# Kernel tuning notes

Measured on AMD Instinct MI355X. Metric: run time of the kernel, lower is better.

The kernel has to match this reference:

```python
import jax, jax.numpy as jnp
import numpy as np

N, DQ, T, H1 = 131072, 256, 4, 512

def setup_inputs() -> dict:
    key = jax.random.key(0)
    k_q, k_w0, k_b0, k_w1, k_z = jax.random.split(key, 5)
    return {
        "q": jax.random.normal(k_q, (N, DQ), dtype=jnp.float32),
        "Z": jax.random.randint(k_z, (N,), 0, T, dtype=jnp.int32),
        "W0": jax.random.normal(k_w0, (T, DQ, H1), dtype=jnp.float32) * (1.0 / np.sqrt(DQ)),
        "b0": jax.random.normal(k_b0, (T, H1), dtype=jnp.float32) * 0.01,
        "W1": jax.random.normal(k_w1, (T, H1), dtype=jnp.float32) * (1.0 / np.sqrt(H1)),
        "b1": jnp.zeros((), dtype=jnp.float32),
    }

def reference(q, Z, W0, b0, W1, b1):
    # Dense grouped-GEMM over all T types (T is small), then select per-atom
    # type result. Avoids materializing the per-atom [N, dq, h1] gathered
    # weight tensor that tf.gather would create.
    h_all = jnp.einsum('nd,tdh->nth', q, W0)              # [N, T, H1]
    h = jnp.take_along_axis(h_all, Z[:, None, None].astype(jnp.int32), axis=1)[:, 0, :]  # [N, H1]
    h = jnp.tanh(h + b0[Z])                               # hidden activations
    F = jnp.einsum('nh,nh->n', h, W1[Z]) + b1             # [N]
    return F
```

## Files before the change

### kernel.cpp

```cpp
#include <hip/hip_runtime.h>
#include <hip/hip_bf16.h>

#define N_ATOMS 131072
#define DQ 256
#define H1 512
#define NTYPES 4
#define TILE_M 64
#define NPAD (N_ATOMS + NTYPES * TILE_M)
#define MTILES ((N_ATOMS / TILE_M) + NTYPES)

typedef __bf16 bf16x8 __attribute__((ext_vector_type(8)));
typedef float f32x16 __attribute__((ext_vector_type(16)));

__device__ __forceinline__ unsigned short f2bf(float f) {
  unsigned int u = __builtin_bit_cast(unsigned int, f);
  u += 0x7fffu + ((u >> 16) & 1u);
  return (unsigned short)(u >> 16);
}

__device__ __forceinline__ float fast_tanh(float x) {
  float e = __expf(2.0f * x);
  return 1.0f - 2.0f * __builtin_amdgcn_rcpf(e + 1.0f);
}

__global__ __launch_bounds__(256) void prep_kernel(
    const float* __restrict__ W0, const int* __restrict__ Z,
    unsigned short* __restrict__ W0s, int* __restrict__ perm,
    int* __restrict__ blockcounts)
{
  const int b = blockIdx.x, tid = threadIdx.x;
  const int gid = b * 256 + tid;

  for (int i = gid; i < NPAD; i += 512 * 256) perm[i] = -1;

  if (gid < NTYPES * (DQ / 8) * H1) {
    const int n  = gid & (H1 - 1);
    const int kg = (gid >> 9) & 31;
    const int t  = gid >> 14;
    const float* src = W0 + ((size_t)(t * DQ + kg * 8) * H1 + n);
    unsigned short o[8];
#pragma unroll
    for (int j = 0; j < 8; ++j) o[j] = f2bf(src[(size_t)j * H1]);
    uint4 v;
    v.x = (unsigned)o[0] | ((unsigned)o[1] << 16);
    v.y = (unsigned)o[2] | ((unsigned)o[3] << 16);
    v.z = (unsigned)o[4] | ((unsigned)o[5] << 16);
    v.w = (unsigned)o[6] | ((unsigned)o[7] << 16);
    ((uint4*)W0s)[gid] = v;
  }

  __shared__ int lc[NTYPES];
  if (tid < NTYPES) lc[tid] = 0;
  __syncthreads();
  atomicAdd(&lc[Z[gid]], 1);
  __syncthreads();
  if (tid < NTYPES) blockcounts[b * NTYPES + tid] = lc[tid];
}

__global__ __launch_bounds__(256) void scan_kernel(
    const int* __restrict__ blockcounts, int* __restrict__ padded_off,
    int* __restrict__ cursors)
{
  __shared__ int sums[NTYPES];
  const int tid = threadIdx.x;
  if (tid < NTYPES) sums[tid] = 0;
  __syncthreads();
  const int t = tid & 3;
  int acc = 0;
  for (int b = tid >> 2; b < 512; b += 64) acc += blockcounts[b * 4 + t];
  atomicAdd(&sums[t], acc);
  __syncthreads();
  if (tid == 0) {
    int off = 0;
#pragma unroll
    for (int i = 0; i < NTYPES; ++i) {
      padded_off[i] = off;
      cursors[i] = off;
      off += (sums[i] + TILE_M - 1) & ~(TILE_M - 1);
    }
    padded_off[NTYPES] = off;
  }
}

__global__ __launch_bounds__(256) void scatter_kernel(
    const int* __restrict__ Z, int* __restrict__ cursors, int* __restrict__ perm)
{
  __shared__ int lc[NTYPES], lbase[NTYPES];
  const int tid = threadIdx.x;
  const int gid = blockIdx.x * 256 + tid;
  if (tid < NTYPES) lc[tid] = 0;
  __syncthreads();
  const int t  = Z[gid];
  const int my = atomicAdd(&lc[t], 1);
  __syncthreads();
  if (tid < NTYPES) lbase[tid] = lc[tid] ? atomicAdd(&cursors[tid], lc[tid]) : 0;
  __syncthreads();
  perm[lbase[t] + my] = gid;
}

__global__ __launch_bounds__(256, 4) void gemm_kernel(
    const float* __restrict__ q, const int* __restrict__ perm,
    const int* __restrict__ padded_off, const unsigned short* __restrict__ W0s,
    const float* __restrict__ b0, const float* __restrict__ W1,
    const float* __restrict__ b1p, float* __restrict__ out)
{
  __shared__ unsigned short Alds[(DQ / 8) * TILE_M * 8];
  __shared__ float Fws[16][TILE_M];

  const int gr0 = blockIdx.x * TILE_M;
  if (gr0 >= padded_off[NTYPES]) return;
  int t = 0;
#pragma unroll
  for (int i = 1; i < NTYPES; ++i) t += (gr0 >= padded_off[i]) ? 1 : 0;

  const int tid = threadIdx.x;

  {
    const int row = tid >> 2, c4 = tid & 3;
    const int atom = perm[gr0 + row];
    const float* qrow = q + (size_t)(atom < 0 ? 0 : atom) * DQ;
#pragma unroll
    for (int i = 0; i < 16; ++i) {
      const int k = c4 * 64 + i * 4;
      float4 v = make_float4(0.f, 0.f, 0.f, 0.f);
      if (atom >= 0) v = *(const float4*)(qrow + k);
      ushort4 o;
      o.x = f2bf(v.x); o.y = f2bf(v.y); o.z = f2bf(v.z); o.w = f2bf(v.w);
      *(ushort4*)&Alds[((k >> 3) * TILE_M + row) * 8 + (k & 7)] = o;
    }
  }
  __syncthreads();

  const int l = tid & 63, w = tid >> 6;
  const int half = l >> 5, ln = l & 31;

  const unsigned short* Bt = W0s + (size_t)t * (DQ * H1);

#pragma unroll
  for (int p = 0; p < 2; ++p) {
    f32x16 acc[2][2];
#pragma unroll
    for (int mt = 0; mt < 2; ++mt)
#pragma unroll
      for (int nt = 0; nt < 2; ++nt) acc[mt][nt] = (f32x16)0.0f;

    const unsigned short* Bbase = Bt + (size_t)(p * 256 + w * 64 + ln) * 8;

#pragma unroll 2
    for (int step = 0; step < 16; ++step) {
      const int kg = 2 * step + half;
      const bf16x8 a0 = *(const bf16x8*)&Alds[(kg * TILE_M + ln) * 8];
      const bf16x8 a1 = *(const bf16x8*)&Alds[(kg * TILE_M + 32 + ln) * 8];
      const unsigned short* bp = Bbase + (size_t)kg * (H1 * 8);
      const bf16x8 bf0 = *(const bf16x8*)(bp);
      const bf16x8 bf1 = *(const bf16x8*)(bp + 32 * 8);
      acc[0][0] = __builtin_amdgcn_mfma_f32_32x32x16_bf16(a0, bf0, acc[0][0], 0, 0, 0);
      acc[1][0] = __builtin_amdgcn_mfma_f32_32x32x16_bf16(a1, bf0, acc[1][0], 0, 0, 0);
      acc[0][1] = __builtin_amdgcn_mfma_f32_32x32x16_bf16(a0, bf1, acc[0][1], 0, 0, 0);
      acc[1][1] = __builtin_amdgcn_mfma_f32_32x32x16_bf16(a1, bf1, acc[1][1], 0, 0, 0);
    }

    float b0v[2], w1v[2];
#pragma unroll
    for (int nt = 0; nt < 2; ++nt) {
      const int c = p * 256 + w * 64 + nt * 32 + ln;
      b0v[nt] = b0[t * H1 + c];
      w1v[nt] = W1[t * H1 + c];
    }
#pragma unroll
    for (int mt = 0; mt < 2; ++mt) {
#pragma unroll
      for (int r = 0; r < 16; ++r) {
        float s = w1v[0] * fast_tanh(acc[mt][0][r] + b0v[0])
                + w1v[1] * fast_tanh(acc[mt][1][r] + b0v[1]);
        s += __shfl_xor(s, 1);
        s += __shfl_xor(s, 2);
        s += __shfl_xor(s, 4);
        if ((l & 7) == 0) {
          const int row  = mt * 32 + (r & 3) + 8 * (r >> 2) + 4 * half;
          const int slot = w * 4 + ((l >> 3) & 3);
          if (p == 0) Fws[slot][row] = s;
          else        Fws[slot][row] += s;
        }
      }
    }
  }
  __syncthreads();

  if (tid < TILE_M) {
    const int atom = perm[gr0 + tid];
    if (atom >= 0) {
      float s = 0.f;
#pragma unroll
      for (int i = 0; i < 16; ++i) s += Fws[i][tid];
      out[atom] = s + b1p[0];
    }
  }
}

extern "C" void kernel_launch(void* const* d_in, const int* in_sizes, int n_in,
                              void* d_out, int out_size, void* d_ws, size_t ws_size,
                              hipStream_t stream) {
  const float* q  = (const float*)d_in[0];
  const int*   Z  = (const int*)d_in[1];
  const float* W0 = (const float*)d_in[2];
  const float* b0 = (const float*)d_in[3];
  const float* W1 = (const float*)d_in[4];
  const float* b1 = (const float*)d_in[5];
  float* out = (float*)d_out;

  char* ws = (char*)d_ws;
  int* blockcounts = (int*)(ws);
  int* padded_off  = (int*)(ws + 8192);
  int* cursors     = (int*)(ws + 8192 + 32);
  int* perm        = (int*)(ws + 8192 + 64);
  unsigned short* W0s = (unsigned short*)(ws + 8192 + 64 + (size_t)NPAD * 4);

  hipLaunchKernelGGL(prep_kernel,    dim3(512),    dim3(256), 0, stream, W0, Z, W0s, perm, blockcounts);
  hipLaunchKernelGGL(scan_kernel,    dim3(1),      dim3(256), 0, stream, blockcounts, padded_off, cursors);
  hipLaunchKernelGGL(scatter_kernel, dim3(512),    dim3(256), 0, stream, Z, cursors, perm);
  hipLaunchKernelGGL(gemm_kernel,    dim3(MTILES), dim3(256), 0, stream, q, perm, padded_off, W0s, b0, W1, b1, out);
}
```

Baseline: 296.0 us.

## Software-pipeline B global loads and A LDS loads across both GEMM passes

Fully unrolls the two N-halves of the grouped GEMM and prefetches B fragments from global memory two k-steps ahead (4-slot register ring) and A fragments from LDS one step ahead. The B loads for the second half are issued during the first half's tail so they overlap the first epilogue. Fws doubles to 32 slots so each half writes partial sums without read-modify-write, and launch bounds drop to 3 waves-per-EU minimum to allow the extra prefetch registers. The cost is higher register pressure, possibly lower occupancy, and more LDS per block.

```diff
diff --git a/kernel.cpp b/kernel.cpp
--- a/kernel.cpp
+++ b/kernel.cpp
@@ -98,14 +98,14 @@
   perm[lbase[t] + my] = gid;
 }
 
-__global__ __launch_bounds__(256, 4) void gemm_kernel(
+__global__ __launch_bounds__(256, 3) void gemm_kernel(
     const float* __restrict__ q, const int* __restrict__ perm,
     const int* __restrict__ padded_off, const unsigned short* __restrict__ W0s,
     const float* __restrict__ b0, const float* __restrict__ W1,
     const float* __restrict__ b1p, float* __restrict__ out)
 {
   __shared__ unsigned short Alds[(DQ / 8) * TILE_M * 8];
-  __shared__ float Fws[16][TILE_M];
+  __shared__ float Fws[32][TILE_M];
 
   const int gr0 = blockIdx.x * TILE_M;
   if (gr0 >= padded_off[NTYPES]) return;
@@ -135,56 +135,91 @@
   const int half = l >> 5, ln = l & 31;
 
   const unsigned short* Bt = W0s + (size_t)t * (DQ * H1);
-
-#pragma unroll
-  for (int p = 0; p < 2; ++p) {
-    f32x16 acc[2][2];
-#pragma unroll
-    for (int mt = 0; mt < 2; ++mt)
-#pragma unroll
-      for (int nt = 0; nt < 2; ++nt) acc[mt][nt] = (f32x16)0.0f;
-
-    const unsigned short* Bbase = Bt + (size_t)(p * 256 + w * 64 + ln) * 8;
-
-#pragma unroll 2
-    for (int step = 0; step < 16; ++step) {
-      const int kg = 2 * step + half;
-      const bf16x8 a0 = *(const bf16x8*)&Alds[(kg * TILE_M + ln) * 8];
-      const bf16x8 a1 = *(const bf16x8*)&Alds[(kg * TILE_M + 32 + ln) * 8];
-      const unsigned short* bp = Bbase + (size_t)kg * (H1 * 8);
-      const bf16x8 bf0 = *(const bf16x8*)(bp);
-      const bf16x8 bf1 = *(const bf16x8*)(bp + 32 * 8);
-      acc[0][0] = __builtin_amdgcn_mfma_f32_32x32x16_bf16(a0, bf0, acc[0][0], 0, 0, 0);
-      acc[1][0] = __builtin_amdgcn_mfma_f32_32x32x16_bf16(a1, bf0, acc[1][0], 0, 0, 0);
-      acc[0][1] = __builtin_amdgcn_mfma_f32_32x32x16_bf16(a0, bf1, acc[0][1], 0, 0, 0);
-      acc[1][1] = __builtin_amdgcn_mfma_f32_32x32x16_bf16(a1, bf1, acc[1][1], 0, 0, 0);
-    }
-
-    float b0v[2], w1v[2];
-#pragma unroll
-    for (int nt = 0; nt < 2; ++nt) {
-      const int c = p * 256 + w * 64 + nt * 32 + ln;
-      b0v[nt] = b0[t * H1 + c];
-      w1v[nt] = W1[t * H1 + c];
-    }
-#pragma unroll
-    for (int mt = 0; mt < 2; ++mt) {
-#pragma unroll
-      for (int r = 0; r < 16; ++r) {
-        float s = w1v[0] * fast_tanh(acc[mt][0][r] + b0v[0])
-                + w1v[1] * fast_tanh(acc[mt][1][r] + b0v[1]);
-        s += __shfl_xor(s, 1);
-        s += __shfl_xor(s, 2);
-        s += __shfl_xor(s, 4);
-        if ((l & 7) == 0) {
-          const int row  = mt * 32 + (r & 3) + 8 * (r >> 2) + 4 * half;
-          const int slot = w * 4 + ((l >> 3) & 3);
-          if (p == 0) Fws[slot][row] = s;
-          else        Fws[slot][row] += s;
-        }
-      }
-    }
-  }
+  const unsigned short* Bb[2] = {
+    Bt + (size_t)(w * 64 + ln) * 8,
+    Bt + (size_t)(256 + w * 64 + ln) * 8
+  };
+
+  bf16x8 bb[4][2];
+  bf16x8 ab[2][2];
+  f32x16 acc[2][2];
+
+#define BISSUE(g) do {                                                        \
+    const int s_ = (g) & 15, p_ = (g) >> 4;                                   \
+    const unsigned short* bp_ = Bb[p_] + (size_t)(2 * s_ + half) * (H1 * 8);  \
+    bb[(g) & 3][0] = *(const bf16x8*)(bp_);                                   \
+    bb[(g) & 3][1] = *(const bf16x8*)(bp_ + 32 * 8);                          \
+  } while (0)
+
+#define AISSUE(g) do {                                                        \
+    const int kg_ = 2 * ((g) & 15) + half;                                    \
+    ab[(g) & 1][0] = *(const bf16x8*)&Alds[(kg_ * TILE_M + ln) * 8];          \
+    ab[(g) & 1][1] = *(const bf16x8*)&Alds[(kg_ * TILE_M + 32 + ln) * 8];     \
+  } while (0)
+
+#define MSTEP(g) do {                                                                          \
+    acc[0][0] = __builtin_amdgcn_mfma_f32_32x32x16_bf16(ab[(g)&1][0], bb[(g)&3][0], acc[0][0], 0, 0, 0); \
+    acc[1][0] = __builtin_amdgcn_mfma_f32_32x32x16_bf16(ab[(g)&1][1], bb[(g)&3][0], acc[1][0], 0, 0, 0); \
+    acc[0][1] = __builtin_amdgcn_mfma_f32_32x32x16_bf16(ab[(g)&1][0], bb[(g)&3][1], acc[0][1], 0, 0, 0); \
+    acc[1][1] = __builtin_amdgcn_mfma_f32_32x32x16_bf16(ab[(g)&1][1], bb[(g)&3][1], acc[1][1], 0, 0, 0); \
+  } while (0)
+
+#define EPILOGUE(p) do {                                                       \
+    float b0v[2], w1v[2];                                                      \
+    _Pragma("unroll")                                                          \
+    for (int nt = 0; nt < 2; ++nt) {                                           \
+      const int c = (p) * 256 + w * 64 + nt * 32 + ln;                         \
+      b0v[nt] = b0[t * H1 + c];                                                \
+      w1v[nt] = W1[t * H1 + c];                                                \
+    }                                                                          \
+    _Pragma("unroll")                                                          \
+    for (int mt = 0; mt < 2; ++mt) {                                           \
+      _Pragma("unroll")                                                        \
+      for (int r = 0; r < 16; ++r) {                                           \
+        float s = w1v[0] * fast_tanh(acc[mt][0][r] + b0v[0])                   \
+                + w1v[1] * fast_tanh(acc[mt][1][r] + b0v[1]);                  \
+        s += __shfl_xor(s, 1);                                                 \
+        s += __shfl_xor(s, 2);                                                 \
+        s += __shfl_xor(s, 4);                                                 \
+        if ((l & 7) == 0) {                                                    \
+          const int row_ = mt * 32 + (r & 3) + 8 * (r >> 2) + 4 * half;        \
+          Fws[(p) * 16 + w * 4 + ((l >> 3) & 3)][row_] = s;                    \
+        }                                                                      \
+      }                                                                        \
+    }                                                                          \
+  } while (0)
+
+#pragma unroll
+  for (int mt = 0; mt < 2; ++mt)
+#pragma unroll
+    for (int nt = 0; nt < 2; ++nt) acc[mt][nt] = (f32x16)0.0f;
+
+  BISSUE(0); BISSUE(1);
+  AISSUE(0);
+#pragma unroll
+  for (int g = 0; g < 14; ++g) { BISSUE(g + 2); AISSUE(g + 1); MSTEP(g); }
+  BISSUE(16); BISSUE(17);
+  AISSUE(15);
+  MSTEP(14); MSTEP(15);
+  EPILOGUE(0);
+
+#pragma unroll
+  for (int mt = 0; mt < 2; ++mt)
+#pragma unroll
+    for (int nt = 0; nt < 2; ++nt) acc[mt][nt] = (f32x16)0.0f;
+
+  AISSUE(16);
+#pragma unroll
+  for (int g = 16; g < 30; ++g) { BISSUE(g + 2); AISSUE(g + 1); MSTEP(g); }
+  AISSUE(31);
+  MSTEP(30); MSTEP(31);
+  EPILOGUE(1);
+
+#undef BISSUE
+#undef AISSUE
+#undef MSTEP
+#undef EPILOGUE
+
   __syncthreads();
 
   if (tid < TILE_M) {
@@ -192,7 +227,7 @@
     if (atom >= 0) {
       float s = 0.f;
 #pragma unroll
-      for (int i = 0; i < 16; ++i) s += Fws[i][tid];
+      for (int i = 0; i < 32; ++i) s += Fws[i][tid];
       out[atom] = s + b1p[0];
     }
   }
```

Result: faster. 285.6 us (-3.5%).
